# Kernel optimization log

Measured on AMD Instinct MI355X. Metric: run time of the kernel, lower is better.

The kernel has to match this reference:

```python
import jax, jax.numpy as jnp
import numpy as np

SIZE = (160, 192, 160)  # matches init_kwargs `size`


def _make_grid(size):
    # torch: meshgrid(arange(s) for s, indexing='ij'), stack last dim, flip last dim
    vecs = [jnp.arange(s, dtype=jnp.float32) for s in size]
    g = jnp.stack(jnp.meshgrid(*vecs, indexing='ij'), axis=-1)
    g = g[..., ::-1]  # last-dim order becomes (x, y, z) = (W, H, D) indices
    return g[None]    # [1, D, H, W, 3]


def _grid_sample_3d(src, locs):
    """Trilinear grid_sample, align_corners=True, padding_mode='zeros'.
    src: [B, C, D, H, W]; locs: [B, D, H, W, 3] in [-1,1], last dim (x,y,z)."""
    B, C, D, H, W = src.shape
    dims_m1 = jnp.array([W - 1, H - 1, D - 1], jnp.float32)
    px = (locs + 1.0) * 0.5 * dims_m1  # unnormalize (align_corners=True)
    x, y, z = px[..., 0], px[..., 1], px[..., 2]
    x0 = jnp.floor(x); y0 = jnp.floor(y); z0 = jnp.floor(z)
    fx, fy, fz = x - x0, y - y0, z - z0
    x0i = x0.astype(jnp.int32); y0i = y0.astype(jnp.int32); z0i = z0.astype(jnp.int32)

    def gather(src_b, iz, iy, ix):  # src_b: [C,D,H,W]; idx: [D,H,W]
        return src_b[:, iz, iy, ix]  # [C,D,H,W]

    out = jnp.zeros(src.shape, src.dtype)
    for dz in (0, 1):
        for dy in (0, 1):
            for dx in (0, 1):
                ix, iy, iz = x0i + dx, y0i + dy, z0i + dz
                valid = (ix >= 0) & (ix < W) & (iy >= 0) & (iy < H) & (iz >= 0) & (iz < D)
                w = ((fx if dx else 1.0 - fx)
                     * (fy if dy else 1.0 - fy)
                     * (fz if dz else 1.0 - fz))
                w = jnp.where(valid, w, 0.0)  # zero padding for OOB
                icx = jnp.clip(ix, 0, W - 1)
                icy = jnp.clip(iy, 0, H - 1)
                icz = jnp.clip(iz, 0, D - 1)
                v = jax.vmap(gather)(src, icz, icy, icx)  # [B,C,D,H,W]
                out = out + w[:, None] * v
    return out


def setup_inputs() -> dict:
    key = jax.random.key(0)
    k1, k2 = jax.random.split(key)
    B, C = 2, 2
    D, H, W = SIZE
    src = jax.random.normal(k1, (B, C, D, H, W), dtype=jnp.float32)
    flow = jax.random.normal(k2, (B, 3, D, H, W), dtype=jnp.float32)
    return {"src": src, "flow": flow}


def reference(src, flow):
    # order='image': no flip of flow channels
    flow = jnp.moveaxis(flow, 1, -1)                      # [B,D,H,W,3]
    grid = _make_grid(SIZE)                                # [1,D,H,W,3]
    s = jnp.array(SIZE, jnp.float32)[::-1] - 1.0           # [W-1,H-1,D-1]
    new_locs = 2.0 * ((grid + flow) / s - 0.5)             # normalized [-1,1]
    return _grid_sample_3d(src, new_locs)
```

## Files before the change

### kernel.cpp

```cpp
#include <hip/hip_runtime.h>

#define DD 160
#define HH 192
#define WW 160
#define SP (DD * HH * WW)
#define NB 2
#define NC 2

#define TX 32
#define TY 8
#define TZ 8
#define RXW 40
#define RYH 15
#define RZD 15
#define REGC (RZD * RYH * RXW)
#define NCHUNK (REGC / 4)
#define NITER 3
#define NTHR 1024

#define NTX 5
#define NTY 24
#define NTZ 20
#define NTILES (NTX * NTY * NTZ * NB)
#define TPX (NTILES / 8)
#define NBLK 512
#define SLOTS (NBLK / 8)

typedef float v2f __attribute__((ext_vector_type(2)));
typedef float v4f __attribute__((ext_vector_type(4)));

typedef const void __attribute__((address_space(1)))* gas_ptr;
typedef void __attribute__((address_space(3)))* las_ptr;

__device__ __forceinline__ v2f ld2_nt(const float* p) {
    return __builtin_nontemporal_load(reinterpret_cast<const v2f*>(p));
}
__device__ __forceinline__ void st2_nt(float* p, v2f v) {
    __builtin_nontemporal_store(v, reinterpret_cast<v2f*>(p));
}
__device__ __forceinline__ v2f ld2g(const float* p) {
    return *reinterpret_cast<const v2f*>(p);
}

__device__ __forceinline__ float sample_global1(
    const float* __restrict__ s,
    int x, int y, int z, float dx, float dy, float dz)
{
    float sx = (float)x + dx, sy = (float)y + dy, sz = (float)z + dz;
    float xf = floorf(sx), yf = floorf(sy), zf = floorf(sz);
    float fx = sx - xf, fy = sy - yf, fz = sz - zf;
    int x0 = (int)xf, y0 = (int)yf, z0 = (int)zf;
    int x1 = x0 + 1, y1 = y0 + 1, z1 = z0 + 1;

    float wx0 = (x0 >= 0 && x0 < WW) ? (1.0f - fx) : 0.0f;
    float wx1 = (x1 >= 0 && x1 < WW) ? fx : 0.0f;
    float wy0 = (y0 >= 0 && y0 < HH) ? (1.0f - fy) : 0.0f;
    float wy1 = (y1 >= 0 && y1 < HH) ? fy : 0.0f;
    float wz0 = (z0 >= 0 && z0 < DD) ? (1.0f - fz) : 0.0f;
    float wz1 = (z1 >= 0 && z1 < DD) ? fz : 0.0f;

    int p  = min(max(x0, 0), WW - 2);
    int i0 = min(max(x0, 0), WW - 1) - p;
    int i1 = min(max(x1, 0), WW - 1) - p;
    int cy0 = min(max(y0, 0), HH - 1), cy1 = min(max(y1, 0), HH - 1);
    int cz0 = min(max(z0, 0), DD - 1), cz1 = min(max(z1, 0), DD - 1);

    int o00 = (cz0 * HH + cy0) * WW + p;
    int o01 = (cz0 * HH + cy1) * WW + p;
    int o10 = (cz1 * HH + cy0) * WW + p;
    int o11 = (cz1 * HH + cy1) * WW + p;

    v2f c00 = ld2g(s + o00);
    v2f c01 = ld2g(s + o01);
    v2f c10 = ld2g(s + o10);
    v2f c11 = ld2g(s + o11);

    #define PICK(v, i) ((i) ? (v).y : (v).x)
    float r;
    r  = (wz0 * wy0) * (wx0 * PICK(c00, i0) + wx1 * PICK(c00, i1));
    r += (wz0 * wy1) * (wx0 * PICK(c01, i0) + wx1 * PICK(c01, i1));
    r += (wz1 * wy0) * (wx0 * PICK(c10, i0) + wx1 * PICK(c10, i1));
    r += (wz1 * wy1) * (wx0 * PICK(c11, i0) + wx1 * PICK(c11, i1));
    #undef PICK
    return r;
}

__device__ __forceinline__ void stage_channel(
    const float* __restrict__ cb, int X0, int Y0, int Z0, int tid, float* sbuf)
{
    #pragma unroll
    for (int i = 0; i < NITER; ++i) {
        int c = tid + i * NTHR;
        if (i < NITER - 1 || c < NCHUNK) {
            int lz  = c / 150;  int r2 = c - lz * 150;
            int ly  = r2 / 10;  int lxc = r2 - ly * 10;
            int mz = min(max(Z0 - 3 + lz, 0), DD - 1);
            int my = min(max(Y0 - 3 + ly, 0), HH - 1);
            int mx = min(max(X0 - 4 + lxc * 4, 0), WW - 4);
            const float* g = cb + (mz * HH + my) * WW + mx;
            __builtin_amdgcn_global_load_lds(
                (gas_ptr)g, (las_ptr)(sbuf + 4 * c), 16, 0, 0);
        }
    }
}

template<bool INTERIOR>
__device__ __forceinline__ float sample_lds(
    const float* __restrict__ sbuf,
    float lx, float ly, float lz, int rx0, int ry0, int rz0)
{
    float xf = floorf(lx), yf = floorf(ly), zf = floorf(lz);
    float fx = lx - xf, fy = ly - yf, fz = lz - zf;
    int ix = (int)xf, iy = (int)yf, iz = (int)zf;

    float wx0, wx1, wy0, wy1, wz0, wz1;
    if (INTERIOR) {
        wx0 = 1.0f - fx; wx1 = fx;
        wy0 = 1.0f - fy; wy1 = fy;
        wz0 = 1.0f - fz; wz1 = fz;
    } else {
        int vx0 = ix + rx0, vy0 = iy + ry0, vz0 = iz + rz0;
        wx0 = (vx0 >= 0  && vx0 < WW)     ? (1.0f - fx) : 0.0f;
        wx1 = (vx0 >= -1 && vx0 < WW - 1) ? fx          : 0.0f;
        wy0 = (vy0 >= 0  && vy0 < HH)     ? (1.0f - fy) : 0.0f;
        wy1 = (vy0 >= -1 && vy0 < HH - 1) ? fy          : 0.0f;
        wz0 = (vz0 >= 0  && vz0 < DD)     ? (1.0f - fz) : 0.0f;
        wz1 = (vz0 >= -1 && vz0 < DD - 1) ? fz          : 0.0f;
    }

    const float* pB = sbuf + (iz * RYH + iy) * RXW + ix;
    float A00 = pB[0],        B00 = pB[1];
    float A01 = pB[RXW],      B01 = pB[RXW + 1];
    const float* pC = pB + RYH * RXW;
    float A10 = pC[0],        B10 = pC[1];
    float A11 = pC[RXW],      B11 = pC[RXW + 1];

    float c00 = wx0 * A00 + wx1 * B00;
    float c01 = wx0 * A01 + wx1 * B01;
    float c10 = wx0 * A10 + wx1 * B10;
    float c11 = wx0 * A11 + wx1 * B11;
    float m0  = wy0 * c00 + wy1 * c01;
    float m1  = wy0 * c10 + wy1 * c11;
    return wz0 * m0 + wz1 * m1;
}

struct Geo {
    int X0, Y0, Z0;
    int x, y, z;
    bool interior;
    const float* sb;
    const float* fp;
    float* op;
};

__device__ __forceinline__ Geo decode_tile(
    int tl, const float* src, const float* flow, float* out,
    int xi, int yl, int zl)
{
    Geo g;
    int tx = tl % NTX;  int t2 = tl / NTX;
    int ty = t2 % NTY;  int t3 = t2 / NTY;
    int tz = t3 % NTZ;  int b  = t3 / NTZ;
    g.X0 = tx * TX; g.Y0 = ty * TY; g.Z0 = tz * TZ;
    g.interior = (tx >= 1) & (tx <= 3) &
                 (ty >= 1) & (ty <= 22) &
                 (tz >= 1) & (tz <= 18);
    g.x = g.X0 + xi; g.y = g.Y0 + yl; g.z = g.Z0 + zl;
    int go = (g.z * HH + g.y) * WW + g.x;
    g.sb = src + b * NC * SP;
    g.fp = flow + b * 3 * SP + go;
    g.op = out + b * NC * SP + go;
    return g;
}

template<bool INTERIOR>
__device__ __forceinline__ void compute_store(
    const float* __restrict__ sbuf, const Geo& g, int cofs,
    v2f dxv, v2f dyv, v2f dzv, int xi, int yl, int zl)
{
    const int rx0 = g.X0 - 4, ry0 = g.Y0 - 3, rz0 = g.Z0 - 3;
    float a[2];
    #pragma unroll
    for (int j = 0; j < 2; ++j) {
        float dx = dxv[j], dy = dyv[j], dz = dzv[j];
        bool inH = (dx >= -4.0f) & (dx < 4.0f) &
                   (dy >= -3.0f) & (dy < 4.0f) &
                   (dz >= -3.0f) & (dz < 4.0f);
        if (inH) {
            float lx = (float)(xi + j + 4) + dx;
            float ly = (float)(yl + 3) + dy;
            float lz = (float)(zl + 3) + dz;
            a[j] = sample_lds<INTERIOR>(sbuf, lx, ly, lz, rx0, ry0, rz0);
        } else {
            a[j] = sample_global1(g.sb + cofs, g.x + j, g.y, g.z, dx, dy, dz);
        }
    }
    v2f o = {a[0], a[1]};
    st2_nt(g.op + cofs, o);
}

__global__ __launch_bounds__(NTHR, 8) void st_warp_kernel(
    const float* __restrict__ src,
    const float* __restrict__ flow,
    float* __restrict__ out)
{
    __shared__ float sA[REGC];
    __shared__ float sB[REGC];

    int u    = blockIdx.x;
    int xcd  = u & 7;
    int slot = u >> 3;
    int tid  = threadIdx.x;

    int xi = (tid & 15) << 1;
    int rr = tid >> 4;
    int yl = rr & 7, zl = rr >> 3;

    int nt = (TPX - slot + SLOTS - 1) / SLOTS;
    int tl = xcd * TPX + slot;

    Geo g = decode_tile(tl, src, flow, out, xi, yl, zl);
    stage_channel(g.sb, g.X0, g.Y0, g.Z0, tid, sA);
    v2f dxv = ld2_nt(g.fp);
    v2f dyv = ld2_nt(g.fp + SP);
    v2f dzv = ld2_nt(g.fp + 2 * SP);

    for (int t = 0; t < nt; ++t) {
        __syncthreads();

        stage_channel(g.sb + SP, g.X0, g.Y0, g.Z0, tid, sB);
        if (g.interior)
            compute_store<true >(sA, g, 0, dxv, dyv, dzv, xi, yl, zl);
        else
            compute_store<false>(sA, g, 0, dxv, dyv, dzv, xi, yl, zl);

        __syncthreads();

        bool more = (t + 1 < nt);
        Geo gn = g;
        v2f nxv = dxv, nyv = dyv, nzv = dzv;
        if (more) {
            gn = decode_tile(tl + (t + 1) * SLOTS, src, flow, out, xi, yl, zl);
            stage_channel(gn.sb, gn.X0, gn.Y0, gn.Z0, tid, sA);
            nxv = ld2_nt(gn.fp);
            nyv = ld2_nt(gn.fp + SP);
            nzv = ld2_nt(gn.fp + 2 * SP);
        }
        if (g.interior)
            compute_store<true >(sB, g, SP, dxv, dyv, dzv, xi, yl, zl);
        else
            compute_store<false>(sB, g, SP, dxv, dyv, dzv, xi, yl, zl);

        g = gn; dxv = nxv; dyv = nyv; dzv = nzv;
    }
}

extern "C" void kernel_launch(void* const* d_in, const int* in_sizes, int n_in,
                              void* d_out, int out_size, void* d_ws, size_t ws_size,
                              hipStream_t stream) {
    const float* src  = (const float*)d_in[0];
    const float* flow = (const float*)d_in[1];
    float* out = (float*)d_out;

    st_warp_kernel<<<NBLK, NTHR, 0, stream>>>(src, flow, out);
}
```

Measured before the change: 279.2 us.

## Interleave both channels in LDS and stage through registers with double buffering

Instead of staging each channel separately with direct global-to-LDS loads, each tile loads both channels into registers and writes them into LDS interleaved as (c0,c1) pairs. Each trilinear sample then reads v2f pairs and computes both channels at once, sharing the index and weight math. The staging buffers double-buffer whole tiles, which leaves one barrier per tile instead of two. LDS use per block doubles, so the block count is halved and launch bounds drop to 4 blocks, and the register staging adds register pressure and VGPR round trips.

```diff
diff --git a/kernel.cpp b/kernel.cpp
--- a/kernel.cpp
+++ b/kernel.cpp
@@ -14,7 +14,7 @@
 #define RYH 15
 #define RZD 15
 #define REGC (RZD * RYH * RXW)
-#define NCHUNK (REGC / 4)
+#define NQUAD (REGC / 4)
 #define NITER 3
 #define NTHR 1024
 
@@ -23,15 +23,12 @@
 #define NTZ 20
 #define NTILES (NTX * NTY * NTZ * NB)
 #define TPX (NTILES / 8)
-#define NBLK 512
+#define NBLK 256
 #define SLOTS (NBLK / 8)
 
 typedef float v2f __attribute__((ext_vector_type(2)));
 typedef float v4f __attribute__((ext_vector_type(4)));
 
-typedef const void __attribute__((address_space(1)))* gas_ptr;
-typedef void __attribute__((address_space(3)))* las_ptr;
-
 __device__ __forceinline__ v2f ld2_nt(const float* p) {
     return __builtin_nontemporal_load(reinterpret_cast<const v2f*>(p));
 }
@@ -41,6 +38,8 @@
 __device__ __forceinline__ v2f ld2g(const float* p) {
     return *reinterpret_cast<const v2f*>(p);
 }
+__device__ __forceinline__ float pick(v2f v, int i) { return i ? v.y : v.x; }
+__device__ __forceinline__ v2f s2(float f) { v2f v = {f, f}; return v; }
 
 __device__ __forceinline__ float sample_global1(
     const float* __restrict__ s,
@@ -75,37 +74,53 @@
     v2f c10 = ld2g(s + o10);
     v2f c11 = ld2g(s + o11);
 
-    #define PICK(v, i) ((i) ? (v).y : (v).x)
     float r;
-    r  = (wz0 * wy0) * (wx0 * PICK(c00, i0) + wx1 * PICK(c00, i1));
-    r += (wz0 * wy1) * (wx0 * PICK(c01, i0) + wx1 * PICK(c01, i1));
-    r += (wz1 * wy0) * (wx0 * PICK(c10, i0) + wx1 * PICK(c10, i1));
-    r += (wz1 * wy1) * (wx0 * PICK(c11, i0) + wx1 * PICK(c11, i1));
-    #undef PICK
+    r  = (wz0 * wy0) * (wx0 * pick(c00, i0) + wx1 * pick(c00, i1));
+    r += (wz0 * wy1) * (wx0 * pick(c01, i0) + wx1 * pick(c01, i1));
+    r += (wz1 * wy0) * (wx0 * pick(c10, i0) + wx1 * pick(c10, i1));
+    r += (wz1 * wy1) * (wx0 * pick(c11, i0) + wx1 * pick(c11, i1));
     return r;
 }
 
-__device__ __forceinline__ void stage_channel(
-    const float* __restrict__ cb, int X0, int Y0, int Z0, int tid, float* sbuf)
+__device__ __forceinline__ void stage_issue(
+    const float* __restrict__ cb, int X0, int Y0, int Z0, int tid,
+    v4f* A, v4f* B, int* ad)
 {
     #pragma unroll
     for (int i = 0; i < NITER; ++i) {
-        int c = tid + i * NTHR;
-        if (i < NITER - 1 || c < NCHUNK) {
-            int lz  = c / 150;  int r2 = c - lz * 150;
-            int ly  = r2 / 10;  int lxc = r2 - ly * 10;
+        int q = tid + i * NTHR;
+        if (i < NITER - 1 || q < NQUAD) {
+            int r  = q / 10;  int xq = q - r * 10;
+            int lz = r / 15;  int ly = r - lz * 15;
             int mz = min(max(Z0 - 3 + lz, 0), DD - 1);
             int my = min(max(Y0 - 3 + ly, 0), HH - 1);
-            int mx = min(max(X0 - 4 + lxc * 4, 0), WW - 4);
-            const float* g = cb + (mz * HH + my) * WW + mx;
-            __builtin_amdgcn_global_load_lds(
-                (gas_ptr)g, (las_ptr)(sbuf + 4 * c), 16, 0, 0);
+            int mx = min(max(X0 - 4 + xq * 4, 0), WW - 4);
+            const float* p = cb + (mz * HH + my) * WW + mx;
+            A[i] = *reinterpret_cast<const v4f*>(p);
+            B[i] = *reinterpret_cast<const v4f*>(p + SP);
+            ad[i] = 8 * q;
+        } else {
+            ad[i] = -1;
+        }
+    }
+}
+
+__device__ __forceinline__ void stage_write(
+    float* __restrict__ sbuf, const v4f* A, const v4f* B, const int* ad)
+{
+    #pragma unroll
+    for (int i = 0; i < NITER; ++i) {
+        if (ad[i] >= 0) {
+            v4f w0 = {A[i].x, B[i].x, A[i].y, B[i].y};
+            v4f w1 = {A[i].z, B[i].z, A[i].w, B[i].w};
+            *reinterpret_cast<v4f*>(&sbuf[ad[i]])     = w0;
+            *reinterpret_cast<v4f*>(&sbuf[ad[i] + 4]) = w1;
         }
     }
 }
 
 template<bool INTERIOR>
-__device__ __forceinline__ float sample_lds(
+__device__ __forceinline__ v2f sample_il(
     const float* __restrict__ sbuf,
     float lx, float ly, float lz, int rx0, int ry0, int rz0)
 {
@@ -128,20 +143,24 @@
         wz1 = (vz0 >= -1 && vz0 < DD - 1) ? fz          : 0.0f;
     }
 
-    const float* pB = sbuf + (iz * RYH + iy) * RXW + ix;
-    float A00 = pB[0],        B00 = pB[1];
-    float A01 = pB[RXW],      B01 = pB[RXW + 1];
-    const float* pC = pB + RYH * RXW;
-    float A10 = pC[0],        B10 = pC[1];
-    float A11 = pC[RXW],      B11 = pC[RXW + 1];
-
-    float c00 = wx0 * A00 + wx1 * B00;
-    float c01 = wx0 * A01 + wx1 * B01;
-    float c10 = wx0 * A10 + wx1 * B10;
-    float c11 = wx0 * A11 + wx1 * B11;
-    float m0  = wy0 * c00 + wy1 * c01;
-    float m1  = wy0 * c10 + wy1 * c11;
-    return wz0 * m0 + wz1 * m1;
+    const float* pB = sbuf + 2 * ((iz * RYH + iy) * RXW + ix);
+    v2f A00 = *(const v2f*)(pB);
+    v2f B00 = *(const v2f*)(pB + 2);
+    v2f A01 = *(const v2f*)(pB + 2 * RXW);
+    v2f B01 = *(const v2f*)(pB + 2 * RXW + 2);
+    const float* pC = pB + 2 * RYH * RXW;
+    v2f A10 = *(const v2f*)(pC);
+    v2f B10 = *(const v2f*)(pC + 2);
+    v2f A11 = *(const v2f*)(pC + 2 * RXW);
+    v2f B11 = *(const v2f*)(pC + 2 * RXW + 2);
+
+    v2f c00 = s2(wx0) * A00 + s2(wx1) * B00;
+    v2f c01 = s2(wx0) * A01 + s2(wx1) * B01;
+    v2f c10 = s2(wx0) * A10 + s2(wx1) * B10;
+    v2f c11 = s2(wx0) * A11 + s2(wx1) * B11;
+    v2f m0  = s2(wy0) * c00 + s2(wy1) * c01;
+    v2f m1  = s2(wy0) * c10 + s2(wy1) * c11;
+    return s2(wz0) * m0 + s2(wz1) * m1;
 }
 
 struct Geo {
@@ -175,11 +194,11 @@
 
 template<bool INTERIOR>
 __device__ __forceinline__ void compute_store(
-    const float* __restrict__ sbuf, const Geo& g, int cofs,
+    const float* __restrict__ sbuf, const Geo& g,
     v2f dxv, v2f dyv, v2f dzv, int xi, int yl, int zl)
 {
     const int rx0 = g.X0 - 4, ry0 = g.Y0 - 3, rz0 = g.Z0 - 3;
-    float a[2];
+    v2f a[2];
     #pragma unroll
     for (int j = 0; j < 2; ++j) {
         float dx = dxv[j], dy = dyv[j], dz = dzv[j];
@@ -190,22 +209,25 @@
             float lx = (float)(xi + j + 4) + dx;
             float ly = (float)(yl + 3) + dy;
             float lz = (float)(zl + 3) + dz;
-            a[j] = sample_lds<INTERIOR>(sbuf, lx, ly, lz, rx0, ry0, rz0);
+            a[j] = sample_il<INTERIOR>(sbuf, lx, ly, lz, rx0, ry0, rz0);
         } else {
-            a[j] = sample_global1(g.sb + cofs, g.x + j, g.y, g.z, dx, dy, dz);
-        }
-    }
-    v2f o = {a[0], a[1]};
-    st2_nt(g.op + cofs, o);
-}
-
-__global__ __launch_bounds__(NTHR, 8) void st_warp_kernel(
+            a[j].x = sample_global1(g.sb,      g.x + j, g.y, g.z, dx, dy, dz);
+            a[j].y = sample_global1(g.sb + SP, g.x + j, g.y, g.z, dx, dy, dz);
+        }
+    }
+    v2f o0 = {a[0].x, a[1].x};
+    v2f o1 = {a[0].y, a[1].y};
+    st2_nt(g.op, o0);
+    st2_nt(g.op + SP, o1);
+}
+
+__global__ __launch_bounds__(NTHR, 4) void st_warp_kernel(
     const float* __restrict__ src,
     const float* __restrict__ flow,
     float* __restrict__ out)
 {
-    __shared__ float sA[REGC];
-    __shared__ float sB[REGC];
+    __shared__ float sX[2 * REGC];
+    __shared__ float sY[2 * REGC];
 
     int u    = blockIdx.x;
     int xcd  = u & 7;
@@ -213,44 +235,46 @@
     int tid  = threadIdx.x;
 
     int xi = (tid & 15) << 1;
-    int rr = tid >> 4;
-    int yl = rr & 7, zl = rr >> 3;
+    int yl = (tid >> 4) & 7;
+    int zl = tid >> 7;
 
     int nt = (TPX - slot + SLOTS - 1) / SLOTS;
     int tl = xcd * TPX + slot;
 
     Geo g = decode_tile(tl, src, flow, out, xi, yl, zl);
-    stage_channel(g.sb, g.X0, g.Y0, g.Z0, tid, sA);
+    v4f A[NITER], B[NITER]; int ad[NITER];
+    stage_issue(g.sb, g.X0, g.Y0, g.Z0, tid, A, B, ad);
     v2f dxv = ld2_nt(g.fp);
     v2f dyv = ld2_nt(g.fp + SP);
     v2f dzv = ld2_nt(g.fp + 2 * SP);
+    stage_write(sX, A, B, ad);
+    __syncthreads();
+
+    float* front = sX;
+    float* back  = sY;
 
     for (int t = 0; t < nt; ++t) {
-        __syncthreads();
-
-        stage_channel(g.sb + SP, g.X0, g.Y0, g.Z0, tid, sB);
-        if (g.interior)
-            compute_store<true >(sA, g, 0, dxv, dyv, dzv, xi, yl, zl);
-        else
-            compute_store<false>(sA, g, 0, dxv, dyv, dzv, xi, yl, zl);
-
-        __syncthreads();
-
         bool more = (t + 1 < nt);
         Geo gn = g;
         v2f nxv = dxv, nyv = dyv, nzv = dzv;
         if (more) {
             gn = decode_tile(tl + (t + 1) * SLOTS, src, flow, out, xi, yl, zl);
-            stage_channel(gn.sb, gn.X0, gn.Y0, gn.Z0, tid, sA);
+            stage_issue(gn.sb, gn.X0, gn.Y0, gn.Z0, tid, A, B, ad);
             nxv = ld2_nt(gn.fp);
             nyv = ld2_nt(gn.fp + SP);
             nzv = ld2_nt(gn.fp + 2 * SP);
         }
+
         if (g.interior)
-            compute_store<true >(sB, g, SP, dxv, dyv, dzv, xi, yl, zl);
+            compute_store<true >(front, g, dxv, dyv, dzv, xi, yl, zl);
         else
-            compute_store<false>(sB, g, SP, dxv, dyv, dzv, xi, yl, zl);
-
+            compute_store<false>(front, g, dxv, dyv, dzv, xi, yl, zl);
+
+        if (more)
+            stage_write(back, A, B, ad);
+
+        __syncthreads();
+        float* tmp = front; front = back; back = tmp;
         g = gn; dxv = nxv; dyv = nyv; dzv = nzv;
     }
 }
```

Result: slower. 319.3 us (+14.4%).
